# Performance work log

Hardware: AMD Instinct MI355X
Metric: run time of the kernel (lower is better)

The kernel has to match this reference:

```python
import jax, jax.numpy as jnp
import numpy as np

CHUNK = 512  # tile size along N; keeps per-step [B,CHUNK,M] tile ~64 MB, never builds full [B,N,M]


def setup_inputs() -> dict:
    key = jax.random.key(0)
    k1, k2 = jax.random.split(key)
    xyz1 = jax.random.normal(k1, (4, 8192, 3), dtype=jnp.float32)
    xyz2 = jax.random.normal(k2, (4, 8192, 3), dtype=jnp.float32)
    return {"xyz1": xyz1, "xyz2": xyz2}


def _chamfer(xyz1, xyz2):
    # xyz1: [B,N,3], xyz2: [B,M,3]
    B, N, _ = xyz1.shape
    M = xyz2.shape[1]
    K = N // CHUNK
    x1_chunks = xyz1.reshape(B, K, CHUNK, 3).transpose(1, 0, 2, 3)  # [K,B,C,3]

    def step(carry, x1k):
        best_d2, best_i2, start = carry  # running mins for xyz2 -> xyz1 direction
        # squared distances for this tile: [B,C,M]
        d = jnp.sum((x1k[:, :, None, :] - xyz2[:, None, :, :]) ** 2, axis=-1)
        # xyz1 -> xyz2: min over M
        d1 = jnp.min(d, axis=2)                              # [B,C]
        i1 = jnp.argmin(d, axis=2).astype(jnp.int32)         # [B,C]
        # xyz2 -> xyz1: partial min over this chunk of N
        dc = jnp.min(d, axis=1)                              # [B,M]
        ic = jnp.argmin(d, axis=1).astype(jnp.int32) + start # [B,M], global index
        upd = dc < best_d2
        best_d2 = jnp.where(upd, dc, best_d2)
        best_i2 = jnp.where(upd, ic, best_i2)
        return (best_d2, best_i2, start + CHUNK), (d1, i1)

    init = (jnp.full((B, M), jnp.inf, dtype=xyz1.dtype),
            jnp.zeros((B, M), dtype=jnp.int32),
            jnp.int32(0))
    (dist2, idx2, _), (d1s, i1s) = jax.lax.scan(step, init, x1_chunks)
    dist1 = d1s.transpose(1, 0, 2).reshape(B, N)
    idx1 = i1s.transpose(1, 0, 2).reshape(B, N)
    return dist1, dist2, idx1, idx2


def reference(xyz1, xyz2):
    # Matches ChamferDistance.forward: (dist1, dist2, idx1, idx2),
    # squared nearest-neighbor distances and int32 argmin indices.
    return _chamfer(xyz1, xyz2)
```

## Files before the change

kernel.cpp:

```cpp
#include <hip/hip_runtime.h>
#include <math.h>


#define QPT 4
#define BLK 256
#define QPB (QPT*BLK)

__global__ __launch_bounds__(256) void chamfer_init(
    unsigned long long* __restrict__ pp, int n)
{
    int i = blockIdx.x * blockDim.x + threadIdx.x;
    if (i < n) pp[i] = ~0ULL;
}

__global__ __launch_bounds__(256, 4) void chamfer_main(
    const float* __restrict__ xyz1, const float* __restrict__ xyz2,
    unsigned long long* __restrict__ pp,
    int N, int M, int B, int S, int C)
{
    const int dir = blockIdx.z;
    const float* q = dir ? xyz2 : xyz1;
    const float* r = dir ? xyz1 : xyz2;
    const int Nq = dir ? M : N;
    const int Nr = dir ? N : M;
    const int b     = blockIdx.y / S;
    const int split = blockIdx.y % S;
    const int base  = split * C;

    extern __shared__ float s[];

    {
        const float4* gv = (const float4*)(r + ((size_t)b * Nr + base) * 3);
        float4* sv = (float4*)s;
        const int elems4 = C * 3 / 4;
        for (int t = threadIdx.x; t < elems4; t += BLK) sv[t] = gv[t];
    }
    __syncthreads();

    float qx[QPT], qy[QPT], qz[QPT];
    int qi[QPT];
    bool qv[QPT];
#pragma unroll
    for (int k = 0; k < QPT; ++k) {
        qi[k] = blockIdx.x * QPB + k * BLK + threadIdx.x;
        qv[k] = qi[k] < Nq;
        const float* qp = q + ((size_t)b * Nq + (qv[k] ? qi[k] : 0)) * 3;
        qx[k] = qp[0]; qy[k] = qp[1]; qz[k] = qp[2];
    }

    float bd[QPT];
    int   gi[QPT];
#pragma unroll
    for (int k = 0; k < QPT; ++k) { bd[k] = INFINITY; gi[k] = 0; }

    const float4* sv = (const float4*)s;
    const int iters = C / 8;
    for (int j8 = 0; j8 < iters; ++j8) {
        float4 f0 = sv[6 * j8 + 0];
        float4 f1 = sv[6 * j8 + 1];
        float4 f2 = sv[6 * j8 + 2];
        float4 f3 = sv[6 * j8 + 3];
        float4 f4 = sv[6 * j8 + 4];
        float4 f5 = sv[6 * j8 + 5];
        float px[8] = { f0.x, f0.w, f1.z, f2.y, f3.x, f3.w, f4.z, f5.y };
        float py[8] = { f0.y, f1.x, f1.w, f2.z, f3.y, f4.x, f4.w, f5.z };
        float pz[8] = { f0.z, f1.y, f2.x, f2.w, f3.z, f4.y, f5.x, f5.w };
#pragma unroll
        for (int k = 0; k < QPT; ++k) {
            float d[8];
#pragma unroll
            for (int p = 0; p < 8; ++p) {
                float dx = qx[k] - px[p];
                float dy = qy[k] - py[p];
                float dz = qz[k] - pz[p];
                d[p] = fmaf(dx, dx, fmaf(dy, dy, dz * dz));
            }
            float m01 = fminf(d[0], d[1]);
            float m23 = fminf(d[2], d[3]);
            float m45 = fminf(d[4], d[5]);
            float m67 = fminf(d[6], d[7]);
            float m = fminf(fminf(m01, m23), fminf(m45, m67));
            if (m < bd[k]) { bd[k] = m; gi[k] = j8; }
        }
    }

    const size_t obase = (size_t)(dir * B + b) * Nq;
#pragma unroll
    for (int k = 0; k < QPT; ++k) {
        if (!qv[k]) continue;
        const int g = gi[k];
        float4 f0 = sv[6 * g + 0];
        float4 f1 = sv[6 * g + 1];
        float4 f2 = sv[6 * g + 2];
        float4 f3 = sv[6 * g + 3];
        float4 f4 = sv[6 * g + 4];
        float4 f5 = sv[6 * g + 5];
        float px[8] = { f0.x, f0.w, f1.z, f2.y, f3.x, f3.w, f4.z, f5.y };
        float py[8] = { f0.y, f1.x, f1.w, f2.z, f3.y, f4.x, f4.w, f5.z };
        float pz[8] = { f0.z, f1.y, f2.x, f2.w, f3.z, f4.y, f5.x, f5.w };
        int best = 0;
#pragma unroll
        for (int p = 7; p >= 0; --p) {
            float dx = qx[k] - px[p];
            float dy = qy[k] - py[p];
            float dz = qz[k] - pz[p];
            float d = fmaf(dx, dx, fmaf(dy, dy, dz * dz));
            if (d == bd[k]) best = p;
        }
        const int idx = base + g * 8 + best;
        unsigned long long packed =
            ((unsigned long long)__float_as_uint(bd[k]) << 32) | (unsigned)idx;
        atomicMin(&pp[obase + qi[k]], packed);
    }
}

__global__ __launch_bounds__(256) void chamfer_final(
    const unsigned long long* __restrict__ pp,
    float* __restrict__ out, int N, int M, int B)
{
    const int gid = blockIdx.x * blockDim.x + threadIdx.x;
    const int perDir0 = B * N;
    int dir, rem;
    if (gid < perDir0) { dir = 0; rem = gid; }
    else if (gid < perDir0 + B * M) { dir = 1; rem = gid - perDir0; }
    else return;
    const int Nq = dir ? M : N;

    unsigned long long v = pp[(size_t)(dir * B) * Nq + rem];

    float* dist_out = out + (dir ? (size_t)B * N : 0);
    float* idx_out  = out + (size_t)B * N + (size_t)B * M + (dir ? (size_t)B * N : 0);
    dist_out[rem] = __uint_as_float((unsigned)(v >> 32));
    idx_out[rem]  = (float)(unsigned)(v & 0xffffffffu);
}

extern "C" void kernel_launch(void* const* d_in, const int* in_sizes, int n_in,
                              void* d_out, int out_size, void* d_ws, size_t ws_size,
                              hipStream_t stream) {
    const float* xyz1 = (const float*)d_in[0];
    const float* xyz2 = (const float*)d_in[1];
    float* out = (float*)d_out;
    const int B = 4;
    const int N = in_sizes[0] / (B * 3);
    const int M = in_sizes[1] / (B * 3);
    const int NQ = (N > M ? N : M);
    const int NR = (N > M ? N : M);

    int S = 32;
    while (NR % (S * 8)) S >>= 1;
    const int C = NR / S;

    unsigned long long* pp = (unsigned long long*)d_ws;
    const int nslots = 2 * B * NQ;

    chamfer_init<<<dim3((nslots + 255) / 256, 1, 1), dim3(256, 1, 1), 0, stream>>>(
        pp, nslots);

    dim3 grid((NQ + QPB - 1) / QPB, B * S, 2);
    size_t lds = (size_t)C * 3 * sizeof(float);
    chamfer_main<<<grid, dim3(BLK, 1, 1), lds, stream>>>(
        xyz1, xyz2, pp, N, M, B, S, C);

    chamfer_final<<<dim3((nslots + 255) / 256, 1, 1), dim3(256, 1, 1), 0, stream>>>(
        pp, out, N, M, B);
}
```

Before: 125.2 us.

## Use expanded-norm distance in inner loop and fuse final pass via last-block counter

The inner loop now computes |p|^2 - 2q·p with per-group precomputed point norms, so each query-point pair costs three FMAs instead of subtractions plus squares. It also tracks a second-best value and falls back to an exact rescan of the whole shared-memory tile when the top two are within an epsilon, to guard against rounding differences in the expanded form. The separate finalize kernel is removed: each block bumps a per-column atomic counter, and the last split block writes the unpacked results, saving one launch. The cost is extra ALU for the second-best tracking, a possibly slow serial rescan for near-ties, and reliance on correct memory ordering between the atomicMin updates and the final atomic loads.

Measured after the change: 293.5 us. 2.34x slower.

```diff
diff --git a/kernel.cpp b/kernel.cpp
--- a/kernel.cpp
+++ b/kernel.cpp
@@ -7,16 +7,18 @@
 #define QPB (QPT*BLK)
 
 __global__ __launch_bounds__(256) void chamfer_init(
-    unsigned long long* __restrict__ pp, int n)
+    unsigned long long* __restrict__ pp, int nslots,
+    unsigned* __restrict__ cnt, int ncols)
 {
     int i = blockIdx.x * blockDim.x + threadIdx.x;
-    if (i < n) pp[i] = ~0ULL;
+    if (i < nslots) pp[i] = ~0ULL;
+    if (i < ncols) cnt[i] = 0u;
 }
 
 __global__ __launch_bounds__(256, 4) void chamfer_main(
     const float* __restrict__ xyz1, const float* __restrict__ xyz2,
-    unsigned long long* __restrict__ pp,
-    int N, int M, int B, int S, int C)
+    unsigned long long* __restrict__ pp, unsigned* __restrict__ cnt,
+    float* __restrict__ out, int N, int M, int B, int S, int C)
 {
     const int dir = blockIdx.z;
     const float* q = dir ? xyz2 : xyz1;
@@ -28,6 +30,7 @@
     const int base  = split * C;
 
     extern __shared__ float s[];
+    __shared__ int lastFlag;
 
     {
         const float4* gv = (const float4*)(r + ((size_t)b * Nr + base) * 3);
@@ -38,6 +41,7 @@
     __syncthreads();
 
     float qx[QPT], qy[QPT], qz[QPT];
+    float n2x[QPT], n2y[QPT], n2z[QPT];
     int qi[QPT];
     bool qv[QPT];
 #pragma unroll
@@ -46,12 +50,13 @@
         qv[k] = qi[k] < Nq;
         const float* qp = q + ((size_t)b * Nq + (qv[k] ? qi[k] : 0)) * 3;
         qx[k] = qp[0]; qy[k] = qp[1]; qz[k] = qp[2];
+        n2x[k] = -2.0f * qx[k]; n2y[k] = -2.0f * qy[k]; n2z[k] = -2.0f * qz[k];
     }
 
-    float bd[QPT];
+    float bd[QPT], bd2[QPT];
     int   gi[QPT];
 #pragma unroll
-    for (int k = 0; k < QPT; ++k) { bd[k] = INFINITY; gi[k] = 0; }
+    for (int k = 0; k < QPT; ++k) { bd[k] = INFINITY; bd2[k] = INFINITY; gi[k] = 0; }
 
     const float4* sv = (const float4*)s;
     const int iters = C / 8;
@@ -65,8 +70,56 @@
         float px[8] = { f0.x, f0.w, f1.z, f2.y, f3.x, f3.w, f4.z, f5.y };
         float py[8] = { f0.y, f1.x, f1.w, f2.z, f3.y, f4.x, f4.w, f5.z };
         float pz[8] = { f0.z, f1.y, f2.x, f2.w, f3.z, f4.y, f5.x, f5.w };
+        float u[8];
+#pragma unroll
+        for (int p = 0; p < 8; ++p)
+            u[p] = fmaf(pz[p], pz[p], fmaf(py[p], py[p], px[p] * px[p]));
 #pragma unroll
         for (int k = 0; k < QPT; ++k) {
+            float t[8];
+#pragma unroll
+            for (int p = 0; p < 8; ++p)
+                t[p] = fmaf(n2x[k], px[p],
+                       fmaf(n2y[k], py[p],
+                       fmaf(n2z[k], pz[p], u[p])));
+            float m = fminf(fminf(fminf(fminf(fminf(fminf(fminf(
+                t[0], t[1]), t[2]), t[3]), t[4]), t[5]), t[6]), t[7]);
+            float old = bd[k];
+            bool c = m < old;
+            bd[k]  = c ? m : old;
+            gi[k]  = c ? j8 : gi[k];
+            bd2[k] = fminf(bd2[k], fmaxf(old, m));
+        }
+    }
+
+    const size_t obase = (size_t)(dir * B + b) * Nq;
+    const float eps = 1e-5f;
+#pragma unroll
+    for (int k = 0; k < QPT; ++k) {
+        if (!qv[k]) continue;
+        unsigned long long packed;
+        if (bd2[k] - bd[k] < eps) {
+            float best = INFINITY; int bidx = 0;
+            for (int j = 0; j < C; ++j) {
+                float dx = qx[k] - s[3 * j + 0];
+                float dy = qy[k] - s[3 * j + 1];
+                float dz = qz[k] - s[3 * j + 2];
+                float d = fmaf(dx, dx, fmaf(dy, dy, dz * dz));
+                if (d < best) { best = d; bidx = j; }
+            }
+            packed = ((unsigned long long)__float_as_uint(best) << 32)
+                   | (unsigned)(base + bidx);
+        } else {
+            const int g = gi[k];
+            float4 f0 = sv[6 * g + 0];
+            float4 f1 = sv[6 * g + 1];
+            float4 f2 = sv[6 * g + 2];
+            float4 f3 = sv[6 * g + 3];
+            float4 f4 = sv[6 * g + 4];
+            float4 f5 = sv[6 * g + 5];
+            float px[8] = { f0.x, f0.w, f1.z, f2.y, f3.x, f3.w, f4.z, f5.y };
+            float py[8] = { f0.y, f1.x, f1.w, f2.z, f3.y, f4.x, f4.w, f5.z };
+            float pz[8] = { f0.z, f1.y, f2.x, f2.w, f3.z, f4.y, f5.x, f5.w };
             float d[8];
 #pragma unroll
             for (int p = 0; p < 8; ++p) {
@@ -75,63 +128,39 @@
                 float dz = qz[k] - pz[p];
                 d[p] = fmaf(dx, dx, fmaf(dy, dy, dz * dz));
             }
-            float m01 = fminf(d[0], d[1]);
-            float m23 = fminf(d[2], d[3]);
-            float m45 = fminf(d[4], d[5]);
-            float m67 = fminf(d[6], d[7]);
-            float m = fminf(fminf(m01, m23), fminf(m45, m67));
-            if (m < bd[k]) { bd[k] = m; gi[k] = j8; }
+            float m = fminf(fminf(fminf(fminf(fminf(fminf(fminf(
+                d[0], d[1]), d[2]), d[3]), d[4]), d[5]), d[6]), d[7]);
+            int best = 0;
+#pragma unroll
+            for (int p = 7; p >= 0; --p)
+                if (d[p] == m) best = p;
+            packed = ((unsigned long long)__float_as_uint(m) << 32)
+                   | (unsigned)(base + g * 8 + best);
+        }
+        atomicMin(&pp[obase + qi[k]], packed);
+    }
+
+    __syncthreads();
+    if (threadIdx.x == 0) {
+        const int col = (dir * B + b) * gridDim.x + blockIdx.x;
+        unsigned old = __hip_atomic_fetch_add(&cnt[col], 1u,
+                          __ATOMIC_ACQ_REL, __HIP_MEMORY_SCOPE_AGENT);
+        lastFlag = (old == (unsigned)(S - 1));
+    }
+    __syncthreads();
+    if (lastFlag) {
+        float* dist_out = out + (dir ? (size_t)B * N : 0);
+        float* idx_out  = out + (size_t)B * N + (size_t)B * M
+                              + (dir ? (size_t)B * N : 0);
+#pragma unroll
+        for (int k = 0; k < QPT; ++k) {
+            if (!qv[k]) continue;
+            unsigned long long v = __hip_atomic_load(&pp[obase + qi[k]],
+                    __ATOMIC_RELAXED, __HIP_MEMORY_SCOPE_AGENT);
+            dist_out[(size_t)b * Nq + qi[k]] = __uint_as_float((unsigned)(v >> 32));
+            idx_out[(size_t)b * Nq + qi[k]]  = (float)(unsigned)(v & 0xffffffffu);
         }
     }
-
-    const size_t obase = (size_t)(dir * B + b) * Nq;
-#pragma unroll
-    for (int k = 0; k < QPT; ++k) {
-        if (!qv[k]) continue;
-        const int g = gi[k];
-        float4 f0 = sv[6 * g + 0];
-        float4 f1 = sv[6 * g + 1];
-        float4 f2 = sv[6 * g + 2];
-        float4 f3 = sv[6 * g + 3];
-        float4 f4 = sv[6 * g + 4];
-        float4 f5 = sv[6 * g + 5];
-        float px[8] = { f0.x, f0.w, f1.z, f2.y, f3.x, f3.w, f4.z, f5.y };
-        float py[8] = { f0.y, f1.x, f1.w, f2.z, f3.y, f4.x, f4.w, f5.z };
-        float pz[8] = { f0.z, f1.y, f2.x, f2.w, f3.z, f4.y, f5.x, f5.w };
-        int best = 0;
-#pragma unroll
-        for (int p = 7; p >= 0; --p) {
-            float dx = qx[k] - px[p];
-            float dy = qy[k] - py[p];
-            float dz = qz[k] - pz[p];
-            float d = fmaf(dx, dx, fmaf(dy, dy, dz * dz));
-            if (d == bd[k]) best = p;
-        }
-        const int idx = base + g * 8 + best;
-        unsigned long long packed =
-            ((unsigned long long)__float_as_uint(bd[k]) << 32) | (unsigned)idx;
-        atomicMin(&pp[obase + qi[k]], packed);
-    }
-}
-
-__global__ __launch_bounds__(256) void chamfer_final(
-    const unsigned long long* __restrict__ pp,
-    float* __restrict__ out, int N, int M, int B)
-{
-    const int gid = blockIdx.x * blockDim.x + threadIdx.x;
-    const int perDir0 = B * N;
-    int dir, rem;
-    if (gid < perDir0) { dir = 0; rem = gid; }
-    else if (gid < perDir0 + B * M) { dir = 1; rem = gid - perDir0; }
-    else return;
-    const int Nq = dir ? M : N;
-
-    unsigned long long v = pp[(size_t)(dir * B) * Nq + rem];
-
-    float* dist_out = out + (dir ? (size_t)B * N : 0);
-    float* idx_out  = out + (size_t)B * N + (size_t)B * M + (dir ? (size_t)B * N : 0);
-    dist_out[rem] = __uint_as_float((unsigned)(v >> 32));
-    idx_out[rem]  = (float)(unsigned)(v & 0xffffffffu);
 }
 
 extern "C" void kernel_launch(void* const* d_in, const int* in_sizes, int n_in,
@@ -152,15 +181,16 @@
 
     unsigned long long* pp = (unsigned long long*)d_ws;
     const int nslots = 2 * B * NQ;
+    const int nqt = (NQ + QPB - 1) / QPB;
+    unsigned* cnt = (unsigned*)((char*)d_ws + (size_t)nslots * 8);
+    const int ncols = 2 * B * nqt;
 
-    chamfer_init<<<dim3((nslots + 255) / 256, 1, 1), dim3(256, 1, 1), 0, stream>>>(
-        pp, nslots);
+    const int initN = (nslots > ncols ? nslots : ncols);
+    chamfer_init<<<dim3((initN + 255) / 256, 1, 1), dim3(256, 1, 1), 0, stream>>>(
+        pp, nslots, cnt, ncols);
 
-    dim3 grid((NQ + QPB - 1) / QPB, B * S, 2);
+    dim3 grid(nqt, B * S, 2);
     size_t lds = (size_t)C * 3 * sizeof(float);
     chamfer_main<<<grid, dim3(BLK, 1, 1), lds, stream>>>(
-        xyz1, xyz2, pp, N, M, B, S, C);
-
-    chamfer_final<<<dim3((nslots + 255) / 256, 1, 1), dim3(256, 1, 1), 0, stream>>>(
-        pp, out, N, M, B);
+        xyz1, xyz2, pp, cnt, out, N, M, B, S, C);
 }
```
